# Performance work log

Measured on AMD Instinct MI355X. Metric: run time of the kernel, lower is better.

## Reference

```python
import jax, jax.numpy as jnp
import numpy as np

N, E, R, C, H = 50000, 800000, 8, 128, 128


def setup_inputs() -> dict:
    key = jax.random.key(0)
    ks = jax.random.split(key, 12)
    s = 0.05
    return {
        "x": jax.random.normal(ks[0], (N, C), jnp.float32),
        "edge_index": jax.random.randint(ks[1], (2, E), 0, N, dtype=jnp.int32),
        "edge_type": jax.random.randint(ks[2], (E,), 0, R, dtype=jnp.int32),
        "W1": jax.random.normal(ks[3], (R, C, H), jnp.float32) * s,
        "root1": jax.random.normal(ks[4], (C, H), jnp.float32) * s,
        "b1": jnp.zeros((H,), jnp.float32),
        "W2": jax.random.normal(ks[5], (R, H, H), jnp.float32) * s,
        "root2": jax.random.normal(ks[6], (H, H), jnp.float32) * s,
        "b2": jnp.zeros((H,), jnp.float32),
        "Wout": jax.random.normal(ks[7], (H, 1), jnp.float32) * s,
        "bout": jnp.zeros((1,), jnp.float32),
    }


def rgcn_conv(x, src, dst, etype, W, root, b):
    # PyG RGCNConv (aggr='mean'): per relation, mean of transformed source
    # features over edges of that relation into the target node, plus root + bias.
    n = x.shape[0]
    num_rel = W.shape[0]
    xs = x[src]  # [E, C] gathered source features (shared across relations)
    out = x @ root + b  # [N, H]
    for r in range(num_rel):  # small fixed relation count -> python loop OK
        m = (etype == r).astype(x.dtype)  # [E]
        sm = jax.ops.segment_sum(xs * m[:, None], dst, num_segments=n)  # [N, C]
        cnt = jax.ops.segment_sum(m, dst, num_segments=n)  # [N]
        agg = sm / jnp.maximum(cnt, 1.0)[:, None]  # mean aggregation
        out = out + agg @ W[r]
    return out


def reference(x, edge_index, edge_type, W1, root1, b1, W2, root2, b2, Wout, bout):
    src, dst = edge_index[0], edge_index[1]
    h = jax.nn.relu(rgcn_conv(x, src, dst, edge_type, W1, root1, b1))
    # dropout is identity in eval mode
    h = jax.nn.relu(rgcn_conv(h, src, dst, edge_type, W2, root2, b2))
    return (h @ Wout + bout)[:, 0]  # squeeze(-1)
```

## Files before the change

kernel.cpp:

```cpp
#include <hip/hip_runtime.h>
#include <hip/hip_bf16.h>


constexpr int NN = 50000;
constexpr int EE = 800000;
constexpr int NB = NN * 8;
constexpr int NCB = (NN + 255) >> 8;
constexpr int EPB = 8192;
constexpr int PBLK = (EE + EPB - 1) / EPB;
constexpr int NSB = 2048;

typedef __attribute__((ext_vector_type(8))) short bf16x8;
typedef __attribute__((ext_vector_type(16))) float f32x16;
typedef __attribute__((address_space(3))) uint32_t lds_u32;
typedef __attribute__((address_space(1))) const uint32_t glb_u32;

static __device__ __forceinline__ ushort f2bf(float f) {
    uint u = __float_as_uint(f);
    uint r = (u + 0x7fffu + ((u >> 16) & 1u)) >> 16;
    return (ushort)r;
}
static __device__ __forceinline__ float bflo(uint v) { return __uint_as_float(v << 16); }
static __device__ __forceinline__ float bfhi(uint v) { return __uint_as_float(v & 0xffff0000u); }

static __device__ __forceinline__ void stage16(const void* g, void* lds) {
    __builtin_amdgcn_global_load_lds((glb_u32*)g, (lds_u32*)lds, 16, 0, 0);
}

__global__ __launch_bounds__(1024) void chist_kernel(const int* __restrict__ dst,
                                                     int* __restrict__ ghist) {
    __shared__ int h[NCB];
    const int t = threadIdx.x;
    for (int i = t; i < NCB; i += 1024) h[i] = 0;
    __syncthreads();
    const int e0 = blockIdx.x * EPB + t;
#pragma unroll
    for (int jj = 0; jj < 8; ++jj) {
        const int e = e0 + jj * 1024;
        if (e < EE) atomicAdd(&h[dst[e] >> 8], 1);
    }
    __syncthreads();
    for (int i = t; i < NCB; i += 1024)
        if (h[i]) atomicAdd(&ghist[i], h[i]);
}

__global__ __launch_bounds__(256) void cscan_kernel(const int* __restrict__ ghist,
                                                    int* __restrict__ gstart,
                                                    int* __restrict__ gcur) {
    __shared__ int sm[256];
    const int t = threadIdx.x;
    const int v = (t < NCB) ? ghist[t] : 0;
    sm[t] = v;
    __syncthreads();
    for (int d = 1; d < 256; d <<= 1) {
        int u = (t >= d) ? sm[t - d] : 0;
        __syncthreads();
        sm[t] += u;
        __syncthreads();
    }
    const int excl = sm[t] - v;
    if (t < NCB) { gstart[t] = excl; gcur[t] = excl; }
    if (t == NCB - 1) gstart[NCB] = excl + v;
}

__global__ __launch_bounds__(1024) void cpart_kernel(const int* __restrict__ src,
                                                     const int* __restrict__ dst,
                                                     const int* __restrict__ et,
                                                     int* __restrict__ gcur,
                                                     uint* __restrict__ packed) {
    __shared__ int h[NCB];
    const int t = threadIdx.x;
    for (int i = t; i < NCB; i += 1024) h[i] = 0;
    __syncthreads();
    const int e0 = blockIdx.x * EPB + t;
    int myb[8]; uint mydat[8];
#pragma unroll
    for (int jj = 0; jj < 8; ++jj) {
        const int e = e0 + jj * 1024;
        if (e < EE) {
            const int d = dst[e];
            myb[jj] = d >> 8;
            mydat[jj] = (uint)src[e] | ((uint)et[e] << 16) | ((uint)(d & 255) << 19);
            atomicAdd(&h[myb[jj]], 1);
        } else myb[jj] = -1;
    }
    __syncthreads();
    for (int i = t; i < NCB; i += 1024)
        h[i] = h[i] ? atomicAdd(&gcur[i], h[i]) : 0;
    __syncthreads();
#pragma unroll
    for (int jj = 0; jj < 8; ++jj) {
        if (myb[jj] >= 0) {
            const int pos = atomicAdd(&h[myb[jj]], 1);
            packed[pos] = mydat[jj];
        }
    }
}

__global__ __launch_bounds__(1024) void fsort_kernel(const int* __restrict__ gstart,
                                                     const uint* __restrict__ packed,
                                                     int* __restrict__ off,
                                                     int* __restrict__ srcs) {
    __shared__ int hist[NSB];
    __shared__ int scn[NSB];
    __shared__ int h2[1024];
    const int b = blockIdx.x;
    const int t = threadIdx.x;
    const int s = gstart[b], e = gstart[b + 1];

    for (int i = t; i < NSB; i += 1024) hist[i] = 0;
    __syncthreads();
    for (int i = s + t; i < e; i += 1024)
        atomicAdd(&hist[(packed[i] >> 16) & 0x7FF], 1);
    __syncthreads();
    const int a0 = hist[2 * t], a1 = hist[2 * t + 1];
    h2[t] = a0 + a1;
    __syncthreads();
    for (int d = 1; d < 1024; d <<= 1) {
        int u = (t >= d) ? h2[t - d] : 0;
        __syncthreads();
        h2[t] += u;
        __syncthreads();
    }
    const int base = h2[t] - (a0 + a1);
    scn[2 * t] = base;
    scn[2 * t + 1] = base + a0;
    __syncthreads();
    const int gsubbase = b << 11;
    for (int i = t; i < NSB; i += 1024) {
        const int g = gsubbase + i;
        if (g < NB) off[g] = s + scn[i];
    }
    if (b == NCB - 1 && t == 0) off[NB] = EE;
    __syncthreads();
    for (int i = s + t; i < e; i += 1024) {
        const uint k = packed[i];
        const int pos = atomicAdd(&scn[(k >> 16) & 0x7FF], 1);
        srcs[s + pos] = (int)(k & 0xFFFF);
    }
}

__global__ __launch_bounds__(256) void cvt_x_kernel(const float* __restrict__ x,
                                                    ushort* __restrict__ xb) {
    const int tid = blockIdx.x * blockDim.x + threadIdx.x;
    const size_t i = (size_t)tid * 8;
    const float4 v0 = *reinterpret_cast<const float4*>(x + i);
    const float4 v1 = *reinterpret_cast<const float4*>(x + i + 4);
    uint4 o;
    o.x = (uint)f2bf(v0.x) | ((uint)f2bf(v0.y) << 16);
    o.y = (uint)f2bf(v0.z) | ((uint)f2bf(v0.w) << 16);
    o.z = (uint)f2bf(v1.x) | ((uint)f2bf(v1.y) << 16);
    o.w = (uint)f2bf(v1.z) | ((uint)f2bf(v1.w) << 16);
    *reinterpret_cast<uint4*>(xb + i) = o;
}

__global__ __launch_bounds__(256) void prep_w_kernel(const float* __restrict__ root1,
                                                     const float* __restrict__ W1,
                                                     const float* __restrict__ root2,
                                                     const float* __restrict__ W2,
                                                     ushort* __restrict__ Bt1,
                                                     ushort* __restrict__ Bt2) {
    const float* root = blockIdx.y ? root2 : root1;
    const float* W    = blockIdx.y ? W2 : W1;
    ushort* Bt        = blockIdx.y ? Bt2 : Bt1;
    const int n = blockIdx.x;
    for (int k = threadIdx.x; k < 1152; k += 256) {
        float v = (k < 128) ? root[(size_t)k * 128 + n]
                            : W[(size_t)(k - 128) * 128 + n];
        Bt[(size_t)n * 1152 + k] = f2bf(v);
    }
}

__global__ __launch_bounds__(256) void agg_kernel(const int* __restrict__ off,
                                                  const int* __restrict__ srcs,
                                                  const ushort* __restrict__ feat,
                                                  ushort* __restrict__ agg) {
    const int wid = (blockIdx.x * blockDim.x + threadIdx.x) >> 6;
    if (wid >= NN) return;
    const int lane = threadIdx.x & 63;
    const int g = lane >> 3;
    const int j = lane & 7;

    const int s1 = off[wid * 8 + g + 1];
    int i = off[wid * 8 + g];
    const int cnt = s1 - i;

    float a[16];
#pragma unroll
    for (int k = 0; k < 16; ++k) a[k] = 0.f;

    int p = (i < s1) ? srcs[i] : 0;
    while (__any(i < s1)) {
        const bool act = i < s1;
        const int pn = (i + 1 < s1) ? srcs[i + 1] : 0;
        if (act) {
            const ushort* row = feat + (size_t)p * 128 + (j << 4);
            const uint4 v0 = reinterpret_cast<const uint4*>(row)[0];
            const uint4 v1 = reinterpret_cast<const uint4*>(row)[1];
            a[0] += bflo(v0.x);  a[1] += bfhi(v0.x);
            a[2] += bflo(v0.y);  a[3] += bfhi(v0.y);
            a[4] += bflo(v0.z);  a[5] += bfhi(v0.z);
            a[6] += bflo(v0.w);  a[7] += bfhi(v0.w);
            a[8] += bflo(v1.x);  a[9] += bfhi(v1.x);
            a[10] += bflo(v1.y); a[11] += bfhi(v1.y);
            a[12] += bflo(v1.z); a[13] += bfhi(v1.z);
            a[14] += bflo(v1.w); a[15] += bfhi(v1.w);
        }
        p = pn;
        ++i;
    }

    const float inv = 1.0f / (float)max(cnt, 1);
    uint4 o0, o1;
    o0.x = (uint)f2bf(a[0] * inv)  | ((uint)f2bf(a[1] * inv)  << 16);
    o0.y = (uint)f2bf(a[2] * inv)  | ((uint)f2bf(a[3] * inv)  << 16);
    o0.z = (uint)f2bf(a[4] * inv)  | ((uint)f2bf(a[5] * inv)  << 16);
    o0.w = (uint)f2bf(a[6] * inv)  | ((uint)f2bf(a[7] * inv)  << 16);
    o1.x = (uint)f2bf(a[8] * inv)  | ((uint)f2bf(a[9] * inv)  << 16);
    o1.y = (uint)f2bf(a[10] * inv) | ((uint)f2bf(a[11] * inv) << 16);
    o1.z = (uint)f2bf(a[12] * inv) | ((uint)f2bf(a[13] * inv) << 16);
    o1.w = (uint)f2bf(a[14] * inv) | ((uint)f2bf(a[15] * inv) << 16);
    ushort* o = agg + (size_t)wid * 1024 + g * 128 + (j << 4);
    reinterpret_cast<uint4*>(o)[0] = o0;
    reinterpret_cast<uint4*>(o)[1] = o1;
}

__global__ __launch_bounds__(256) void gemm_mfma(const ushort* __restrict__ xb,
                                                 const ushort* __restrict__ agg,
                                                 const ushort* __restrict__ Bt,
                                                 const float* __restrict__ bias,
                                                 ushort* __restrict__ hout) {
    __shared__ __align__(16) uint8_t smem[49152];
    const int t = threadIdx.x;
    const int lane = t & 63;
    const int w = t >> 6;
    const int wr = w >> 1, wc = w & 1;
    const int n0 = blockIdx.x * 64;
    const int l31 = lane & 31;
    const int lhalf = lane >> 5;

    f32x16 acc0, acc1;
#pragma unroll
    for (int r = 0; r < 16; ++r) { acc0[r] = 0.f; acc1[r] = 0.f; }

    const int rA = wr * 32 + l31;
    const int aoff = rA * 128, aswz = (rA & 7) << 4;
    const int nB0 = wc * 64 + l31;
    const int nB1 = nB0 + 32;
    const int boff0 = 8192 + nB0 * 128, bswz0 = (nB0 & 7) << 4;
    const int boff1 = 8192 + nB1 * 128, bswz1 = (nB1 & 7) << 4;
    const int ckb = lhalf << 4;

    const int rsub = lane >> 3;
    const int srcChunk = (((lane & 7) ^ (lane >> 3)) << 4);
    int garowA[2];
#pragma unroll
    for (int jj = 0; jj < 2; ++jj)
        garowA[jj] = min(n0 + 16 * w + 8 * jj + rsub, NN - 1);
    size_t bOffG[4];
#pragma unroll
    for (int jj = 0; jj < 4; ++jj)
        bOffG[jj] = (size_t)(32 * w + 8 * jj + rsub) * 2304 + srcChunk;

    const uint8_t* xb8  = (const uint8_t*)xb;
    const uint8_t* agg8 = (const uint8_t*)agg;
    const uint8_t* Bt8  = (const uint8_t*)Bt;

    auto STAGE = [&](int buf, int kt) {
        uint8_t* base = smem + buf * 24576;
        const uint8_t* Asrc; int shift, koffB;
        if (kt < 2) { Asrc = xb8;  shift = 8;  koffB = kt * 128; }
        else        { Asrc = agg8; shift = 11; koffB = (kt - 2) * 128; }
#pragma unroll
        for (int jj = 0; jj < 2; ++jj)
            stage16(Asrc + (((size_t)garowA[jj]) << shift) + koffB + srcChunk,
                    base + (2 * w + jj) * 1024);
#pragma unroll
        for (int jj = 0; jj < 4; ++jj)
            stage16(Bt8 + bOffG[jj] + kt * 128,
                    base + 8192 + (4 * w + jj) * 1024);
    };

    auto COMPUTE = [&](int buf) {
        const uint8_t* base = smem + buf * 24576;
#pragma unroll
        for (int kb = 0; kb < 4; ++kb) {
            const int cb = kb * 32 + ckb;
            const bf16x8 af = *reinterpret_cast<const bf16x8*>(base + aoff  + (cb ^ aswz));
            const bf16x8 b0 = *reinterpret_cast<const bf16x8*>(base + boff0 + (cb ^ bswz0));
            const bf16x8 b1 = *reinterpret_cast<const bf16x8*>(base + boff1 + (cb ^ bswz1));
            acc0 = __builtin_amdgcn_mfma_f32_32x32x16_bf16(af, b0, acc0, 0, 0, 0);
            acc1 = __builtin_amdgcn_mfma_f32_32x32x16_bf16(af, b1, acc1, 0, 0, 0);
        }
    };

    STAGE(0, 0);
    __syncthreads();
    int cur = 0;
#pragma unroll 1
    for (int kt = 0; kt < 17; ++kt) {
        STAGE(cur ^ 1, kt + 1);
        COMPUTE(cur);
        __syncthreads();
        cur ^= 1;
    }
    COMPUTE(cur);

#pragma unroll
    for (int ni = 0; ni < 2; ++ni) {
        const int col = wc * 64 + ni * 32 + l31;
        const float bv = bias[col];
        const f32x16& a = ni ? acc1 : acc0;
#pragma unroll
        for (int reg = 0; reg < 16; ++reg) {
            const int row = n0 + wr * 32 + 4 * lhalf + (reg & 3) + 8 * (reg >> 2);
            if (row < NN) {
                const float v = fmaxf(a[reg] + bv, 0.f);
                hout[(size_t)row * 128 + col] = f2bf(v);
            }
        }
    }
}

__global__ __launch_bounds__(256) void out_kernel(const ushort* __restrict__ h2,
                                                  const float* __restrict__ Wout,
                                                  const float* __restrict__ bout,
                                                  float* __restrict__ outp) {
    const int wid = (blockIdx.x * blockDim.x + threadIdx.x) >> 6;
    if (wid >= NN) return;
    const int lane = threadIdx.x & 63;
    const uint v = *reinterpret_cast<const uint*>(h2 + (size_t)wid * 128 + (lane << 1));
    const float2 ww = *reinterpret_cast<const float2*>(Wout + (lane << 1));
    float s = fmaf(bflo(v), ww.x, bfhi(v) * ww.y);
#pragma unroll
    for (int d = 32; d > 0; d >>= 1) s += __shfl_down(s, d, 64);
    if (lane == 0) outp[wid] = s + bout[0];
}

extern "C" void kernel_launch(void* const* d_in, const int* in_sizes, int n_in,
                              void* d_out, int out_size, void* d_ws, size_t ws_size,
                              hipStream_t stream) {
    const float* x     = (const float*)d_in[0];
    const int*   eidx  = (const int*)  d_in[1];
    const int*   etype = (const int*)  d_in[2];
    const float* W1    = (const float*)d_in[3];
    const float* root1 = (const float*)d_in[4];
    const float* b1    = (const float*)d_in[5];
    const float* W2    = (const float*)d_in[6];
    const float* root2 = (const float*)d_in[7];
    const float* b2    = (const float*)d_in[8];
    const float* Wout  = (const float*)d_in[9];
    const float* bout  = (const float*)d_in[10];
    float* out = (float*)d_out;

    const int* src = eidx;
    const int* dst = eidx + EE;

    char* ws = (char*)d_ws;
    size_t pos = 0;
    auto take = [&](size_t bytes) {
        char* p = ws + pos;
        pos = (pos + bytes + 255) & ~(size_t)255;
        return p;
    };
    int*    ghist  = (int*)   take((size_t)NCB * 4);
    int*    gstart = (int*)   take((size_t)(NCB + 1) * 4);
    int*    gcur   = (int*)   take((size_t)NCB * 4);
    uint*   packed = (uint*)  take((size_t)EE * 4);
    int*    off    = (int*)   take((size_t)(NB + 1) * 4);
    int*    srcs   = (int*)   take((size_t)EE * 4);
    ushort* xb     = (ushort*)take((size_t)NN * 128 * 2);
    ushort* h1     = (ushort*)take((size_t)NN * 128 * 2);
    ushort* h2     = (ushort*)take((size_t)NN * 128 * 2);
    ushort* agg    = (ushort*)take((size_t)NN * 1024 * 2);
    ushort* Bt1    = (ushort*)take((size_t)128 * 1152 * 2);
    ushort* Bt2    = (ushort*)take((size_t)128 * 1152 * 2);
    (void)ws_size; (void)n_in; (void)in_sizes; (void)out_size;

    const int wblocks = (NN + 3) / 4;
    const int gblocks = (NN + 63) / 64;

    hipMemsetAsync(ghist, 0, (size_t)NCB * 4, stream);
    chist_kernel<<<PBLK, 1024, 0, stream>>>(dst, ghist);
    cscan_kernel<<<1, 256, 0, stream>>>(ghist, gstart, gcur);
    cpart_kernel<<<PBLK, 1024, 0, stream>>>(src, dst, etype, gcur, packed);
    fsort_kernel<<<NCB, 1024, 0, stream>>>(gstart, packed, off, srcs);
    prep_w_kernel<<<dim3(128, 2), 256, 0, stream>>>(root1, W1, root2, W2, Bt1, Bt2);
    cvt_x_kernel <<<3125, 256, 0, stream>>>(x, xb);

    agg_kernel<<<wblocks, 256, 0, stream>>>(off, srcs, xb, agg);
    gemm_mfma <<<gblocks, 256, 0, stream>>>(xb, agg, Bt1, b1, h1);
    agg_kernel<<<wblocks, 256, 0, stream>>>(off, srcs, h1, agg);
    gemm_mfma <<<gblocks, 256, 0, stream>>>(h1, agg, Bt2, b2, h2);
    out_kernel<<<wblocks, 256, 0, stream>>>(h2, Wout, bout, out);
}
```

Baseline: 217.1 us.

## Fuse per-relation mean aggregation into MFMA GEMM, drop agg buffer

Replaces the separate aggregation kernel and GEMM with one kernel that, per relation, gathers and averages neighbour features into shared memory and immediately runs the MFMA over that K-slice. This removes the write and re-read of the large per-relation aggregate buffer and two launches. In exchange the gather is done by 4 threads per node in a serial loop with less latency hiding, and the GEMM loses its double-buffered pipeline, serialising gather and compute with extra barriers.

```diff
diff --git a/kernel.cpp b/kernel.cpp
--- a/kernel.cpp
+++ b/kernel.cpp
@@ -171,65 +171,12 @@
     }
 }
 
-__global__ __launch_bounds__(256) void agg_kernel(const int* __restrict__ off,
+__global__ __launch_bounds__(256) void gemm_fused(const ushort* __restrict__ feat,
+                                                  const int* __restrict__ off,
                                                   const int* __restrict__ srcs,
-                                                  const ushort* __restrict__ feat,
-                                                  ushort* __restrict__ agg) {
-    const int wid = (blockIdx.x * blockDim.x + threadIdx.x) >> 6;
-    if (wid >= NN) return;
-    const int lane = threadIdx.x & 63;
-    const int g = lane >> 3;
-    const int j = lane & 7;
-
-    const int s1 = off[wid * 8 + g + 1];
-    int i = off[wid * 8 + g];
-    const int cnt = s1 - i;
-
-    float a[16];
-#pragma unroll
-    for (int k = 0; k < 16; ++k) a[k] = 0.f;
-
-    int p = (i < s1) ? srcs[i] : 0;
-    while (__any(i < s1)) {
-        const bool act = i < s1;
-        const int pn = (i + 1 < s1) ? srcs[i + 1] : 0;
-        if (act) {
-            const ushort* row = feat + (size_t)p * 128 + (j << 4);
-            const uint4 v0 = reinterpret_cast<const uint4*>(row)[0];
-            const uint4 v1 = reinterpret_cast<const uint4*>(row)[1];
-            a[0] += bflo(v0.x);  a[1] += bfhi(v0.x);
-            a[2] += bflo(v0.y);  a[3] += bfhi(v0.y);
-            a[4] += bflo(v0.z);  a[5] += bfhi(v0.z);
-            a[6] += bflo(v0.w);  a[7] += bfhi(v0.w);
-            a[8] += bflo(v1.x);  a[9] += bfhi(v1.x);
-            a[10] += bflo(v1.y); a[11] += bfhi(v1.y);
-            a[12] += bflo(v1.z); a[13] += bfhi(v1.z);
-            a[14] += bflo(v1.w); a[15] += bfhi(v1.w);
-        }
-        p = pn;
-        ++i;
-    }
-
-    const float inv = 1.0f / (float)max(cnt, 1);
-    uint4 o0, o1;
-    o0.x = (uint)f2bf(a[0] * inv)  | ((uint)f2bf(a[1] * inv)  << 16);
-    o0.y = (uint)f2bf(a[2] * inv)  | ((uint)f2bf(a[3] * inv)  << 16);
-    o0.z = (uint)f2bf(a[4] * inv)  | ((uint)f2bf(a[5] * inv)  << 16);
-    o0.w = (uint)f2bf(a[6] * inv)  | ((uint)f2bf(a[7] * inv)  << 16);
-    o1.x = (uint)f2bf(a[8] * inv)  | ((uint)f2bf(a[9] * inv)  << 16);
-    o1.y = (uint)f2bf(a[10] * inv) | ((uint)f2bf(a[11] * inv) << 16);
-    o1.z = (uint)f2bf(a[12] * inv) | ((uint)f2bf(a[13] * inv) << 16);
-    o1.w = (uint)f2bf(a[14] * inv) | ((uint)f2bf(a[15] * inv) << 16);
-    ushort* o = agg + (size_t)wid * 1024 + g * 128 + (j << 4);
-    reinterpret_cast<uint4*>(o)[0] = o0;
-    reinterpret_cast<uint4*>(o)[1] = o1;
-}
-
-__global__ __launch_bounds__(256) void gemm_mfma(const ushort* __restrict__ xb,
-                                                 const ushort* __restrict__ agg,
-                                                 const ushort* __restrict__ Bt,
-                                                 const float* __restrict__ bias,
-                                                 ushort* __restrict__ hout) {
+                                                  const ushort* __restrict__ Bt,
+                                                  const float* __restrict__ bias,
+                                                  ushort* __restrict__ hout) {
     __shared__ __align__(16) uint8_t smem[49152];
     const int t = threadIdx.x;
     const int lane = t & 63;
@@ -244,67 +191,99 @@
     for (int r = 0; r < 16; ++r) { acc0[r] = 0.f; acc1[r] = 0.f; }
 
     const int rA = wr * 32 + l31;
-    const int aoff = rA * 128, aswz = (rA & 7) << 4;
-    const int nB0 = wc * 64 + l31;
-    const int nB1 = nB0 + 32;
-    const int boff0 = 8192 + nB0 * 128, bswz0 = (nB0 & 7) << 4;
-    const int boff1 = 8192 + nB1 * 128, bswz1 = (nB1 & 7) << 4;
+    const int aoff = rA * 256, aswz = (rA & 7) << 4;
+    const int nB0 = wc * 64 + l31, nB1 = nB0 + 32;
+    const int boff0 = 16384 + nB0 * 256, bswz0 = (nB0 & 7) << 4;
+    const int boff1 = 16384 + nB1 * 256, bswz1 = (nB1 & 7) << 4;
     const int ckb = lhalf << 4;
 
-    const int rsub = lane >> 3;
-    const int srcChunk = (((lane & 7) ^ (lane >> 3)) << 4);
-    int garowA[2];
-#pragma unroll
-    for (int jj = 0; jj < 2; ++jj)
-        garowA[jj] = min(n0 + 16 * w + 8 * jj + rsub, NN - 1);
-    size_t bOffG[4];
-#pragma unroll
-    for (int jj = 0; jj < 4; ++jj)
-        bOffG[jj] = (size_t)(32 * w + 8 * jj + rsub) * 2304 + srcChunk;
-
-    const uint8_t* xb8  = (const uint8_t*)xb;
-    const uint8_t* agg8 = (const uint8_t*)agg;
-    const uint8_t* Bt8  = (const uint8_t*)Bt;
-
-    auto STAGE = [&](int buf, int kt) {
-        uint8_t* base = smem + buf * 24576;
-        const uint8_t* Asrc; int shift, koffB;
-        if (kt < 2) { Asrc = xb8;  shift = 8;  koffB = kt * 128; }
-        else        { Asrc = agg8; shift = 11; koffB = (kt - 2) * 128; }
-#pragma unroll
-        for (int jj = 0; jj < 2; ++jj)
-            stage16(Asrc + (((size_t)garowA[jj]) << shift) + koffB + srcChunk,
-                    base + (2 * w + jj) * 1024);
-#pragma unroll
-        for (int jj = 0; jj < 4; ++jj)
-            stage16(Bt8 + bOffG[jj] + kt * 128,
-                    base + 8192 + (4 * w + jj) * 1024);
+    const int gi = t >> 2, gj = t & 3;
+    const int gnode = min(n0 + gi, NN - 1);
+    int offs[9];
+#pragma unroll
+    for (int r = 0; r < 9; ++r) offs[r] = off[gnode * 8 + r];
+
+    const int srow = lane >> 4;
+    const int schunk = lane & 15;
+
+    const uint8_t* feat8 = (const uint8_t*)feat;
+    const uint8_t* Bt8   = (const uint8_t*)Bt;
+
+    auto STAGE_B = [&](int kt) {
+#pragma unroll
+        for (int jj = 0; jj < 8; ++jj) {
+            const int n = w * 32 + jj * 4 + srow;
+            stage16(Bt8 + (size_t)n * 2304 + kt * 256 + ((schunk ^ (n & 7)) << 4),
+                    smem + 16384 + (w * 32 + jj * 4) * 256 + (size_t)0 );
+        }
     };
-
-    auto COMPUTE = [&](int buf) {
-        const uint8_t* base = smem + buf * 24576;
-#pragma unroll
-        for (int kb = 0; kb < 4; ++kb) {
+    auto STAGE_A0 = [&]() {
+#pragma unroll
+        for (int jj = 0; jj < 4; ++jj) {
+            const int lr = w * 16 + jj * 4 + srow;
+            const int gr = min(n0 + lr, NN - 1);
+            stage16(feat8 + (size_t)gr * 256 + ((schunk ^ (lr & 7)) << 4),
+                    smem + (w * 16 + jj * 4) * 256);
+        }
+    };
+
+    auto COMPUTE = [&]() {
+#pragma unroll
+        for (int kb = 0; kb < 8; ++kb) {
             const int cb = kb * 32 + ckb;
-            const bf16x8 af = *reinterpret_cast<const bf16x8*>(base + aoff  + (cb ^ aswz));
-            const bf16x8 b0 = *reinterpret_cast<const bf16x8*>(base + boff0 + (cb ^ bswz0));
-            const bf16x8 b1 = *reinterpret_cast<const bf16x8*>(base + boff1 + (cb ^ bswz1));
+            const bf16x8 af = *reinterpret_cast<const bf16x8*>(smem + aoff  + (cb ^ aswz));
+            const bf16x8 b0 = *reinterpret_cast<const bf16x8*>(smem + boff0 + (cb ^ bswz0));
+            const bf16x8 b1 = *reinterpret_cast<const bf16x8*>(smem + boff1 + (cb ^ bswz1));
             acc0 = __builtin_amdgcn_mfma_f32_32x32x16_bf16(af, b0, acc0, 0, 0, 0);
             acc1 = __builtin_amdgcn_mfma_f32_32x32x16_bf16(af, b1, acc1, 0, 0, 0);
         }
     };
 
-    STAGE(0, 0);
-    __syncthreads();
-    int cur = 0;
-#pragma unroll 1
-    for (int kt = 0; kt < 17; ++kt) {
-        STAGE(cur ^ 1, kt + 1);
-        COMPUTE(cur);
-        __syncthreads();
-        cur ^= 1;
-    }
-    COMPUTE(cur);
+    STAGE_A0();
+    STAGE_B(0);
+    __syncthreads();
+    COMPUTE();
+    __syncthreads();
+
+#pragma unroll
+    for (int r = 0; r < 8; ++r) {
+        STAGE_B(r + 1);
+        {
+            const int s = offs[r], e = offs[r + 1];
+            float a[32];
+#pragma unroll
+            for (int k = 0; k < 32; ++k) a[k] = 0.f;
+            int p = (s < e) ? srcs[s] : 0;
+            for (int i = s; i < e; ++i) {
+                const int pn = (i + 1 < e) ? srcs[i + 1] : 0;
+                const uint4* rp = reinterpret_cast<const uint4*>(
+                    feat8 + (size_t)p * 256 + (gj << 6));
+                const uint4 q0 = rp[0], q1 = rp[1], q2 = rp[2], q3 = rp[3];
+                const uint u[16] = { q0.x,q0.y,q0.z,q0.w, q1.x,q1.y,q1.z,q1.w,
+                                     q2.x,q2.y,q2.z,q2.w, q3.x,q3.y,q3.z,q3.w };
+#pragma unroll
+                for (int m = 0; m < 16; ++m) {
+                    a[2 * m]     += bflo(u[m]);
+                    a[2 * m + 1] += bfhi(u[m]);
+                }
+                p = pn;
+            }
+            const float inv = 1.0f / (float)max(e - s, 1);
+            uint o[16];
+#pragma unroll
+            for (int m = 0; m < 16; ++m)
+                o[m] = (uint)f2bf(a[2 * m] * inv) | ((uint)f2bf(a[2 * m + 1] * inv) << 16);
+#pragma unroll
+            for (int m = 0; m < 4; ++m) {
+                const int chunk = (4 * gj + m) ^ (gi & 7);
+                *reinterpret_cast<uint4*>(smem + gi * 256 + chunk * 16) =
+                    make_uint4(o[4 * m], o[4 * m + 1], o[4 * m + 2], o[4 * m + 3]);
+            }
+        }
+        __syncthreads();
+        COMPUTE();
+        __syncthreads();
+    }
 
 #pragma unroll
     for (int ni = 0; ni < 2; ++ni) {
@@ -372,7 +351,6 @@
     ushort* xb     = (ushort*)take((size_t)NN * 128 * 2);
     ushort* h1     = (ushort*)take((size_t)NN * 128 * 2);
     ushort* h2     = (ushort*)take((size_t)NN * 128 * 2);
-    ushort* agg    = (ushort*)take((size_t)NN * 1024 * 2);
     ushort* Bt1    = (ushort*)take((size_t)128 * 1152 * 2);
     ushort* Bt2    = (ushort*)take((size_t)128 * 1152 * 2);
     (void)ws_size; (void)n_in; (void)in_sizes; (void)out_size;
@@ -388,9 +366,7 @@
     prep_w_kernel<<<dim3(128, 2), 256, 0, stream>>>(root1, W1, root2, W2, Bt1, Bt2);
     cvt_x_kernel <<<3125, 256, 0, stream>>>(x, xb);
 
-    agg_kernel<<<wblocks, 256, 0, stream>>>(off, srcs, xb, agg);
-    gemm_mfma <<<gblocks, 256, 0, stream>>>(xb, agg, Bt1, b1, h1);
-    agg_kernel<<<wblocks, 256, 0, stream>>>(off, srcs, h1, agg);
-    gemm_mfma <<<gblocks, 256, 0, stream>>>(h1, agg, Bt2, b2, h2);
+    gemm_fused<<<gblocks, 256, 0, stream>>>(xb, off, srcs, Bt1, b1, h1);
+    gemm_fused<<<gblocks, 256, 0, stream>>>(h1, off, srcs, Bt2, b2, h2);
     out_kernel<<<wblocks, 256, 0, stream>>>(h2, Wout, bout, out);
 }
```

Result: slower. 252.6 us (+16.3%).

## Split GEMM columns across blocks and use three-stage vmcnt-gated LDS pipeline

Applied to the files above, without the earlier changes.

The MFMA GEMM now covers 64 output columns per block, using a 2-D grid over column and row tiles. This halves the B staging and the accumulator registers per block. The LDS pipeline moves from double buffering with __syncthreads to a three-buffer ring that waits on vmcnt before a raw s_barrier, so two stages of loads stay in flight during compute. The cost is that each A tile is read by two blocks, which relies on L2 hits when the paired column blocks run close together, and total block count doubles.

```diff
diff --git a/kernel.cpp b/kernel.cpp
--- a/kernel.cpp
+++ b/kernel.cpp
@@ -235,89 +235,85 @@
     const int lane = t & 63;
     const int w = t >> 6;
     const int wr = w >> 1, wc = w & 1;
-    const int n0 = blockIdx.x * 64;
+    const int n0 = blockIdx.y * 64;
+    const int c0 = blockIdx.x * 64;
     const int l31 = lane & 31;
     const int lhalf = lane >> 5;
 
-    f32x16 acc0, acc1;
-#pragma unroll
-    for (int r = 0; r < 16; ++r) { acc0[r] = 0.f; acc1[r] = 0.f; }
+    f32x16 acc;
+#pragma unroll
+    for (int r = 0; r < 16; ++r) acc[r] = 0.f;
 
     const int rA = wr * 32 + l31;
     const int aoff = rA * 128, aswz = (rA & 7) << 4;
-    const int nB0 = wc * 64 + l31;
-    const int nB1 = nB0 + 32;
-    const int boff0 = 8192 + nB0 * 128, bswz0 = (nB0 & 7) << 4;
-    const int boff1 = 8192 + nB1 * 128, bswz1 = (nB1 & 7) << 4;
+    const int nB = wc * 32 + l31;
+    const int boff = 8192 + nB * 128, bswz = (nB & 7) << 4;
     const int ckb = lhalf << 4;
 
     const int rsub = lane >> 3;
     const int srcChunk = (((lane & 7) ^ (lane >> 3)) << 4);
-    int garowA[2];
-#pragma unroll
-    for (int jj = 0; jj < 2; ++jj)
-        garowA[jj] = min(n0 + 16 * w + 8 * jj + rsub, NN - 1);
-    size_t bOffG[4];
-#pragma unroll
-    for (int jj = 0; jj < 4; ++jj)
-        bOffG[jj] = (size_t)(32 * w + 8 * jj + rsub) * 2304 + srcChunk;
+    int garowA[2]; size_t bOffG[2]; int ldsOff[2];
+#pragma unroll
+    for (int jj = 0; jj < 2; ++jj) {
+        const int id = 2 * w + jj;
+        garowA[jj] = min(n0 + id * 8 + rsub, NN - 1);
+        bOffG[jj]  = (size_t)(c0 + id * 8 + rsub) * 2304 + srcChunk;
+        ldsOff[jj] = id * 1024;
+    }
 
     const uint8_t* xb8  = (const uint8_t*)xb;
     const uint8_t* agg8 = (const uint8_t*)agg;
     const uint8_t* Bt8  = (const uint8_t*)Bt;
 
     auto STAGE = [&](int buf, int kt) {
-        uint8_t* base = smem + buf * 24576;
+        uint8_t* base = smem + buf * 16384;
         const uint8_t* Asrc; int shift, koffB;
         if (kt < 2) { Asrc = xb8;  shift = 8;  koffB = kt * 128; }
         else        { Asrc = agg8; shift = 11; koffB = (kt - 2) * 128; }
 #pragma unroll
         for (int jj = 0; jj < 2; ++jj)
             stage16(Asrc + (((size_t)garowA[jj]) << shift) + koffB + srcChunk,
-                    base + (2 * w + jj) * 1024);
-#pragma unroll
-        for (int jj = 0; jj < 4; ++jj)
+                    base + ldsOff[jj]);
+#pragma unroll
+        for (int jj = 0; jj < 2; ++jj)
             stage16(Bt8 + bOffG[jj] + kt * 128,
-                    base + 8192 + (4 * w + jj) * 1024);
+                    base + 8192 + ldsOff[jj]);
     };
 
     auto COMPUTE = [&](int buf) {
-        const uint8_t* base = smem + buf * 24576;
+        const uint8_t* base = smem + buf * 16384;
 #pragma unroll
         for (int kb = 0; kb < 4; ++kb) {
             const int cb = kb * 32 + ckb;
-            const bf16x8 af = *reinterpret_cast<const bf16x8*>(base + aoff  + (cb ^ aswz));
-            const bf16x8 b0 = *reinterpret_cast<const bf16x8*>(base + boff0 + (cb ^ bswz0));
-            const bf16x8 b1 = *reinterpret_cast<const bf16x8*>(base + boff1 + (cb ^ bswz1));
-            acc0 = __builtin_amdgcn_mfma_f32_32x32x16_bf16(af, b0, acc0, 0, 0, 0);
-            acc1 = __builtin_amdgcn_mfma_f32_32x32x16_bf16(af, b1, acc1, 0, 0, 0);
+            const bf16x8 af = *reinterpret_cast<const bf16x8*>(base + aoff + (cb ^ aswz));
+            const bf16x8 bf = *reinterpret_cast<const bf16x8*>(base + boff + (cb ^ bswz));
+            acc = __builtin_amdgcn_mfma_f32_32x32x16_bf16(af, bf, acc, 0, 0, 0);
         }
     };
 
     STAGE(0, 0);
-    __syncthreads();
-    int cur = 0;
+    STAGE(1, 1);
 #pragma unroll 1
     for (int kt = 0; kt < 17; ++kt) {
-        STAGE(cur ^ 1, kt + 1);
-        COMPUTE(cur);
-        __syncthreads();
-        cur ^= 1;
-    }
-    COMPUTE(cur);
-
-#pragma unroll
-    for (int ni = 0; ni < 2; ++ni) {
-        const int col = wc * 64 + ni * 32 + l31;
-        const float bv = bias[col];
-        const f32x16& a = ni ? acc1 : acc0;
-#pragma unroll
-        for (int reg = 0; reg < 16; ++reg) {
-            const int row = n0 + wr * 32 + 4 * lhalf + (reg & 3) + 8 * (reg >> 2);
-            if (row < NN) {
-                const float v = fmaxf(a[reg] + bv, 0.f);
-                hout[(size_t)row * 128 + col] = f2bf(v);
-            }
+        asm volatile("s_waitcnt vmcnt(4)" ::: "memory");
+        __builtin_amdgcn_sched_barrier(0);
+        __builtin_amdgcn_s_barrier();
+        COMPUTE(kt % 3);
+        if (kt < 16) STAGE((kt + 2) % 3, kt + 2);
+    }
+    asm volatile("s_waitcnt vmcnt(0)" ::: "memory");
+    __builtin_amdgcn_sched_barrier(0);
+    __builtin_amdgcn_s_barrier();
+    COMPUTE(17 % 3);
+
+    const int col = c0 + wc * 32 + l31;
+    const float bv = bias[col - c0 + c0];
+#pragma unroll
+    for (int reg = 0; reg < 16; ++reg) {
+        const int row = n0 + wr * 32 + 4 * lhalf + (reg & 3) + 8 * (reg >> 2);
+        if (row < NN) {
+            const float v = fmaxf(acc[reg] + bv, 0.f);
+            hout[(size_t)row * 128 + col] = f2bf(v);
         }
     }
 }
@@ -378,7 +374,7 @@
     (void)ws_size; (void)n_in; (void)in_sizes; (void)out_size;
 
     const int wblocks = (NN + 3) / 4;
-    const int gblocks = (NN + 63) / 64;
+    const dim3 ggrid(2, (NN + 63) / 64);
 
     hipMemsetAsync(ghist, 0, (size_t)NCB * 4, stream);
     chist_kernel<<<PBLK, 1024, 0, stream>>>(dst, ghist);
@@ -389,8 +385,8 @@
     cvt_x_kernel <<<3125, 256, 0, stream>>>(x, xb);
 
     agg_kernel<<<wblocks, 256, 0, stream>>>(off, srcs, xb, agg);
-    gemm_mfma <<<gblocks, 256, 0, stream>>>(xb, agg, Bt1, b1, h1);
+    gemm_mfma <<<ggrid, 256, 0, stream>>>(xb, agg, Bt1, b1, h1);
     agg_kernel<<<wblocks, 256, 0, stream>>>(off, srcs, h1, agg);
-    gemm_mfma <<<gblocks, 256, 0, stream>>>(h1, agg, Bt2, b2, h2);
+    gemm_mfma <<<ggrid, 256, 0, stream>>>(h1, agg, Bt2, b2, h2);
     out_kernel<<<wblocks, 256, 0, stream>>>(h2, Wout, bout, out);
 }
```

Measured after the change: 227.4 us. 1.05x slower.
